# Kernel optimization log

Measured on AMD Instinct MI355X. Metric: run time of the kernel, lower is better.

Reference implementation:

```python
import jax, jax.numpy as jnp
import numpy as np

N_NODES = 100000
NODE_DIM = 64
IN_DIM_V = 128
N_LAYERS = 4
N_CLASSES = 40
N_EDGES = 1600000
LEAKY_SLOPE = 0.2
BN_EPS = 1e-5


def setup_inputs() -> dict:
    key = jax.random.key(0)
    ks = jax.random.split(key, 12)
    V = jax.random.normal(ks[0], (N_NODES, IN_DIM_V), dtype=jnp.float32)
    src = jax.random.randint(ks[1], (N_EDGES,), 0, N_NODES, dtype=jnp.int64 if jax.config.jax_enable_x64 else jnp.int32)
    dst = jax.random.randint(ks[2], (N_EDGES,), 0, N_NODES, dtype=jnp.int64 if jax.config.jax_enable_x64 else jnp.int32)
    s_in = 1.0 / np.sqrt(IN_DIM_V)
    s_h = 1.0 / np.sqrt(NODE_DIM)
    W_in = jax.random.normal(ks[3], (IN_DIM_V, NODE_DIM), dtype=jnp.float32) * s_in
    b_in = jnp.zeros((NODE_DIM,), jnp.float32)
    W_l = jax.random.normal(ks[4], (N_LAYERS, NODE_DIM, NODE_DIM), dtype=jnp.float32) * s_h
    b_l = jnp.zeros((N_LAYERS, NODE_DIM), jnp.float32)
    gamma = jnp.ones((N_LAYERS, NODE_DIM), jnp.float32)
    beta = jnp.zeros((N_LAYERS, NODE_DIM), jnp.float32)
    W_out = jax.random.normal(ks[5], (NODE_DIM, N_CLASSES), dtype=jnp.float32) * s_h
    b_out = jnp.zeros((N_CLASSES,), jnp.float32)
    return {"V": V, "src": src, "dst": dst, "W_in": W_in, "b_in": b_in,
            "W_l": W_l, "b_l": b_l, "gamma": gamma, "beta": beta,
            "W_out": W_out, "b_out": b_out}


def _batchnorm(x, g, b):
    # BatchNorm1d in training mode: biased variance over the node axis
    m = jnp.mean(x, axis=0)
    v = jnp.mean(jnp.square(x - m), axis=0)
    return (x - m) * jax.lax.rsqrt(v + BN_EPS) * g + b


def reference(V, src, dst, W_in, b_in, W_l, b_l, gamma, beta, W_out, b_out):
    N = V.shape[0]
    ones = jnp.ones((src.shape[0],), V.dtype)
    deg_out = jax.ops.segment_sum(ones, src, num_segments=N)
    deg_in = jax.ops.segment_sum(ones, dst, num_segments=N)
    norm_src = jax.lax.rsqrt(jnp.clip(deg_out, 1.0))[:, None]  # [N,1]
    norm_dst = jax.lax.rsqrt(jnp.clip(deg_in, 1.0))[:, None]

    # trans_input: linear embedding in_dim_V -> node_dim
    h = V @ W_in + b_in  # [N, node_dim]

    for l in range(N_LAYERS):
        h_in = h
        # dropout p=0 / eval mode -> identity
        # GraphConv norm='both': D^{-1/2} A D^{-1/2} X W + b
        m = h * norm_src                                      # [N, d]
        agg = jax.ops.segment_sum(m[src], dst, num_segments=N)  # gather-scatter over edges
        agg = agg * norm_dst
        hc = agg @ W_l[l] + b_l[l]
        hc = _batchnorm(hc, gamma[l], beta[l])
        hc = jnp.where(hc >= 0, hc, LEAKY_SLOPE * hc)
        h = hc + h_in  # residual (cell index hard-wired to 1 in source)

    logits = h @ W_out + b_out  # trans_output: node_dim -> n_classes
    return jax.nn.log_softmax(logits, axis=1)
```

## Files before the change

### kernel.cpp

```cpp
#include <hip/hip_runtime.h>
#include <math.h>


#define LEAKY_SLOPE 0.2f
#define BN_EPS 1e-5f
#define DEG_CAP 48

__device__ __forceinline__ unsigned short f2bf(float f) {
  unsigned int x = __float_as_uint(f);
  unsigned int r = (x + 0x7FFFu + ((x >> 16) & 1u)) >> 16;
  return (unsigned short)r;
}
__device__ __forceinline__ float bf2f(unsigned short u) {
  return __uint_as_float((unsigned int)u << 16);
}

__global__ __launch_bounds__(256, 8)
void hist_kernel(const int* __restrict__ src, int* __restrict__ cnt_src, int E, int N) {
  int bid = blockIdx.x;
  int w = bid & 7;
  int chunk = (N + 7) >> 3;
  int lo = w * chunk;
  int hi = min(lo + chunk, N);
  int i = (bid >> 3) * blockDim.x + threadIdx.x;
  int stride = (gridDim.x >> 3) * blockDim.x;
  for (; i < E; i += stride) {
    int s = src[i];
    if (s >= lo && s < hi) atomicAdd(&cnt_src[s], 1);
  }
}

__global__ __launch_bounds__(256, 8)
void fill_kernel(const int* __restrict__ src, const int* __restrict__ dst,
                 int* __restrict__ cnt_dst, int* __restrict__ bucket, int E, int N) {
  int bid = blockIdx.x;
  int w = bid & 7;
  int chunk = (N + 7) >> 3;
  int lo = w * chunk;
  int hi = min(lo + chunk, N);
  int i = (bid >> 3) * blockDim.x + threadIdx.x;
  int stride = (gridDim.x >> 3) * blockDim.x;
  for (; i < E; i += stride) {
    int d = dst[i];
    if (d >= lo && d < hi) {
      int pos = atomicAdd(&cnt_dst[d], 1);
      if (pos < DEG_CAP) bucket[d * DEG_CAP + pos] = src[i];
    }
  }
}

__global__ __launch_bounds__(256, 8)
void norms_kernel(const int* __restrict__ cnt_src, const int* __restrict__ cnt_dst,
                  float* __restrict__ norm_src, float* __restrict__ norm_dst, int N) {
  int i = blockIdx.x * blockDim.x + threadIdx.x;
  if (i < N) {
    norm_src[i] = rsqrtf(fmaxf((float)cnt_src[i], 1.0f));
    norm_dst[i] = rsqrtf(fmaxf((float)cnt_dst[i], 1.0f));
  }
}

__global__ __launch_bounds__(256) __attribute__((amdgpu_waves_per_eu(3, 4)))
void input_gemm_kernel(const float* __restrict__ V, const float* __restrict__ W_in,
                       const float* __restrict__ b_in, const float* __restrict__ norm_src,
                       float* __restrict__ h, unsigned short* __restrict__ hs, int N) {
  __shared__ __align__(16) float sW[128][64];
  __shared__ __align__(16) float sA[32][132];
  int tid = threadIdx.x;
  int c0 = (tid & 15) * 4;
  int rp = tid >> 4;
  int base = blockIdx.x * 32;

  float4 b4 = *(const float4*)&b_in[c0];

  #pragma unroll
  for (int it = 0; it < 8; it++) {
    int i = tid + it * 256;
    int r = i >> 4, cc = (i & 15) * 4;
    *(float4*)&sW[r][cc] = *(const float4*)&W_in[r * 64 + cc];
  }
  #pragma unroll
  for (int it = 0; it < 4; it++) {
    int i = tid + it * 256;
    int r = i >> 5, cc = (i & 31) * 4;
    int n = base + r;
    float4 v = make_float4(0.f, 0.f, 0.f, 0.f);
    if (n < N) v = *(const float4*)&V[(size_t)n * 128 + cc];
    *(float4*)&sA[r][cc] = v;
  }
  __syncthreads();

  int r0 = rp * 2, r1 = rp * 2 + 1;
  float acc0[4] = {0.f, 0.f, 0.f, 0.f};
  float acc1[4] = {0.f, 0.f, 0.f, 0.f};
  #pragma unroll 4
  for (int d0 = 0; d0 < 128; d0 += 4) {
    float4 wr0 = *(const float4*)&sW[d0 + 0][c0];
    float4 wr1 = *(const float4*)&sW[d0 + 1][c0];
    float4 wr2 = *(const float4*)&sW[d0 + 2][c0];
    float4 wr3 = *(const float4*)&sW[d0 + 3][c0];
    float4 a0 = *(const float4*)&sA[r0][d0];
    float4 a1 = *(const float4*)&sA[r1][d0];
    acc0[0] += a0.x * wr0.x + a0.y * wr1.x + a0.z * wr2.x + a0.w * wr3.x;
    acc0[1] += a0.x * wr0.y + a0.y * wr1.y + a0.z * wr2.y + a0.w * wr3.y;
    acc0[2] += a0.x * wr0.z + a0.y * wr1.z + a0.z * wr2.z + a0.w * wr3.z;
    acc0[3] += a0.x * wr0.w + a0.y * wr1.w + a0.z * wr2.w + a0.w * wr3.w;
    acc1[0] += a1.x * wr0.x + a1.y * wr1.x + a1.z * wr2.x + a1.w * wr3.x;
    acc1[1] += a1.x * wr0.y + a1.y * wr1.y + a1.z * wr2.y + a1.w * wr3.y;
    acc1[2] += a1.x * wr0.z + a1.y * wr1.z + a1.z * wr2.z + a1.w * wr3.z;
    acc1[3] += a1.x * wr0.w + a1.y * wr1.w + a1.z * wr2.w + a1.w * wr3.w;
  }

  int n0 = base + r0, n1 = base + r1;
  if (n0 < N) {
    float4 o = make_float4(acc0[0] + b4.x, acc0[1] + b4.y, acc0[2] + b4.z, acc0[3] + b4.w);
    *(float4*)&h[(size_t)n0 * 64 + c0] = o;
    float ns = norm_src[n0];
    ushort4 s = make_ushort4(f2bf(o.x * ns), f2bf(o.y * ns), f2bf(o.z * ns), f2bf(o.w * ns));
    *(ushort4*)&hs[(size_t)n0 * 64 + c0] = s;
  }
  if (n1 < N) {
    float4 o = make_float4(acc1[0] + b4.x, acc1[1] + b4.y, acc1[2] + b4.z, acc1[3] + b4.w);
    *(float4*)&h[(size_t)n1 * 64 + c0] = o;
    float ns = norm_src[n1];
    ushort4 s = make_ushort4(f2bf(o.x * ns), f2bf(o.y * ns), f2bf(o.z * ns), f2bf(o.w * ns));
    *(ushort4*)&hs[(size_t)n1 * 64 + c0] = s;
  }
}

__global__ __launch_bounds__(256, 8)
void agg_kernel(const unsigned short* __restrict__ hs, const float* __restrict__ norm_dst,
                const int* __restrict__ cnt_dst, const int* __restrict__ bucket,
                float* __restrict__ agg, int N) {
  int wid = __builtin_amdgcn_readfirstlane(blockIdx.x * 4 + (threadIdx.x >> 6));
  int lane = threadIdx.x & 63;
  if (wid >= N) return;
  int len = cnt_dst[wid];
  float nd = norm_dst[wid];
  const int* bkt = bucket + wid * DEG_CAP;
  float a0=0.f,a1=0.f,a2=0.f,a3=0.f,a4=0.f,a5=0.f,a6=0.f,a7=0.f;
  for (int j = 0; j < len; j += 8) {
    int s0=0,s1=0,s2=0,s3=0,s4=0,s5=0,s6=0,s7=0;
    if (j + 0 < len) s0 = bkt[j + 0];
    if (j + 1 < len) s1 = bkt[j + 1];
    if (j + 2 < len) s2 = bkt[j + 2];
    if (j + 3 < len) s3 = bkt[j + 3];
    if (j + 4 < len) s4 = bkt[j + 4];
    if (j + 5 < len) s5 = bkt[j + 5];
    if (j + 6 < len) s6 = bkt[j + 6];
    if (j + 7 < len) s7 = bkt[j + 7];
    unsigned short h0=0,h1=0,h2=0,h3=0,h4=0,h5=0,h6=0,h7=0;
    if (j + 0 < len) h0 = hs[(size_t)s0 * 64 + lane];
    if (j + 1 < len) h1 = hs[(size_t)s1 * 64 + lane];
    if (j + 2 < len) h2 = hs[(size_t)s2 * 64 + lane];
    if (j + 3 < len) h3 = hs[(size_t)s3 * 64 + lane];
    if (j + 4 < len) h4 = hs[(size_t)s4 * 64 + lane];
    if (j + 5 < len) h5 = hs[(size_t)s5 * 64 + lane];
    if (j + 6 < len) h6 = hs[(size_t)s6 * 64 + lane];
    if (j + 7 < len) h7 = hs[(size_t)s7 * 64 + lane];
    if (j + 0 < len) a0 += bf2f(h0);
    if (j + 1 < len) a1 += bf2f(h1);
    if (j + 2 < len) a2 += bf2f(h2);
    if (j + 3 < len) a3 += bf2f(h3);
    if (j + 4 < len) a4 += bf2f(h4);
    if (j + 5 < len) a5 += bf2f(h5);
    if (j + 6 < len) a6 += bf2f(h6);
    if (j + 7 < len) a7 += bf2f(h7);
  }
  float acc = ((a0 + a1) + (a2 + a3)) + ((a4 + a5) + (a6 + a7));
  agg[(size_t)wid * 64 + lane] = acc * nd;
}

__global__ __launch_bounds__(256) __attribute__((amdgpu_waves_per_eu(4, 4)))
void gemm_stats_kernel(const float* __restrict__ agg, const float* __restrict__ W,
                       const float* __restrict__ b, float* __restrict__ hc,
                       float* __restrict__ stats, int N) {
  __shared__ __align__(16) float sW[64][64];
  __shared__ __align__(16) float sA[64][68];
  int tid = threadIdx.x;
  int lane = tid & 63;
  int wv = tid >> 6;
  int cg = lane & 15;
  int ng = lane >> 4;
  int nrow0 = wv * 16 + ng * 4;
  int base = blockIdx.x * 64;

  #pragma unroll
  for (int it = 0; it < 4; it++) {
    int i = tid + it * 256;
    int r = i >> 4, c4 = (i & 15) * 4;
    *(float4*)&sW[r][c4] = *(const float4*)&W[r * 64 + c4];
  }
  #pragma unroll
  for (int it = 0; it < 4; it++) {
    int i = tid + it * 256;
    int r = i >> 4, c4 = (i & 15) * 4;
    int n = base + r;
    float4 v = make_float4(0.f, 0.f, 0.f, 0.f);
    if (n < N) v = *(const float4*)&agg[(size_t)n * 64 + c4];
    *(float4*)&sA[r][c4] = v;
  }
  __syncthreads();

  float4 b4 = *(const float4*)&b[cg * 4];

  float acc[4][4];
  #pragma unroll
  for (int i = 0; i < 4; i++)
    #pragma unroll
    for (int c = 0; c < 4; c++) acc[i][c] = 0.f;

  #pragma unroll 4
  for (int d0 = 0; d0 < 64; d0 += 4) {
    float4 wr0 = *(const float4*)&sW[d0 + 0][cg * 4];
    float4 wr1 = *(const float4*)&sW[d0 + 1][cg * 4];
    float4 wr2 = *(const float4*)&sW[d0 + 2][cg * 4];
    float4 wr3 = *(const float4*)&sW[d0 + 3][cg * 4];
    #pragma unroll
    for (int i = 0; i < 4; i++) {
      float4 av = *(const float4*)&sA[nrow0 + i][d0];
      acc[i][0] += av.x * wr0.x + av.y * wr1.x + av.z * wr2.x + av.w * wr3.x;
      acc[i][1] += av.x * wr0.y + av.y * wr1.y + av.z * wr2.y + av.w * wr3.y;
      acc[i][2] += av.x * wr0.z + av.y * wr1.z + av.z * wr2.z + av.w * wr3.z;
      acc[i][3] += av.x * wr0.w + av.y * wr1.w + av.z * wr2.w + av.w * wr3.w;
    }
  }

  float st_s0=0.f,st_s1=0.f,st_s2=0.f,st_s3=0.f;
  float st_q0=0.f,st_q1=0.f,st_q2=0.f,st_q3=0.f;
  #pragma unroll
  for (int i = 0; i < 4; i++) {
    int n = base + nrow0 + i;
    if (n < N) {
      float4 o;
      o.x = acc[i][0] + b4.x; o.y = acc[i][1] + b4.y;
      o.z = acc[i][2] + b4.z; o.w = acc[i][3] + b4.w;
      *(float4*)&hc[(size_t)n * 64 + cg * 4] = o;
      st_s0 += o.x; st_s1 += o.y; st_s2 += o.z; st_s3 += o.w;
      st_q0 += o.x * o.x; st_q1 += o.y * o.y;
      st_q2 += o.z * o.z; st_q3 += o.w * o.w;
    }
  }

  __syncthreads();
  int rr = wv * 4 + ng;
  *(float4*)&sA[rr][cg * 4]      = make_float4(st_s0, st_s1, st_s2, st_s3);
  *(float4*)&sA[16 + rr][cg * 4] = make_float4(st_q0, st_q1, st_q2, st_q3);
  __syncthreads();
  if (tid < 64) {
    float s = 0.f, q = 0.f;
    #pragma unroll
    for (int r = 0; r < 16; r++) { s += sA[r][tid]; q += sA[16 + r][tid]; }
    atomicAdd(&stats[tid], s);
    atomicAdd(&stats[64 + tid], q);
  }
}

__global__ __launch_bounds__(256, 8)
void apply_kernel(const float* __restrict__ hc, const float* __restrict__ stats,
                  const float* __restrict__ gamma, const float* __restrict__ beta,
                  const float* __restrict__ norm_src, float* __restrict__ h,
                  unsigned short* __restrict__ hs, int N, int write_hs) {
  __shared__ float s_scale[64];
  __shared__ float s_shift[64];
  int tid = threadIdx.x;
  if (tid < 64) {
    float s = stats[tid];
    float ss = stats[64 + tid];
    float invN = 1.0f / (float)N;
    float mean = s * invN;
    float var = fmaxf(ss * invN - mean * mean, 0.0f);
    float scale = gamma[tid] * rsqrtf(var + BN_EPS);
    s_scale[tid] = scale;
    s_shift[tid] = beta[tid] - mean * scale;
  }
  __syncthreads();
  int total4 = N * 16;
  int i = blockIdx.x * blockDim.x + threadIdx.x;
  int stride = gridDim.x * blockDim.x;
  for (; i < total4; i += stride) {
    float4 v = ((const float4*)hc)[i];
    float4 r = ((const float4*)h)[i];
    int cb = (i * 4) & 63;
    int n = i >> 4;
    float o0 = v.x * s_scale[cb + 0] + s_shift[cb + 0];
    float o1 = v.y * s_scale[cb + 1] + s_shift[cb + 1];
    float o2 = v.z * s_scale[cb + 2] + s_shift[cb + 2];
    float o3 = v.w * s_scale[cb + 3] + s_shift[cb + 3];
    o0 = (o0 >= 0.f) ? o0 : LEAKY_SLOPE * o0;
    o1 = (o1 >= 0.f) ? o1 : LEAKY_SLOPE * o1;
    o2 = (o2 >= 0.f) ? o2 : LEAKY_SLOPE * o2;
    o3 = (o3 >= 0.f) ? o3 : LEAKY_SLOPE * o3;
    float4 oh;
    oh.x = o0 + r.x; oh.y = o1 + r.y; oh.z = o2 + r.z; oh.w = o3 + r.w;
    ((float4*)h)[i] = oh;
    if (write_hs) {
      float nsc = norm_src[n];
      ushort4 os = make_ushort4(f2bf(oh.x * nsc), f2bf(oh.y * nsc),
                                f2bf(oh.z * nsc), f2bf(oh.w * nsc));
      ((ushort4*)hs)[i] = os;
    }
  }
}

__global__ __launch_bounds__(256, 4)
void out_kernel(const float* __restrict__ h, const float* __restrict__ W_out,
                const float* __restrict__ b_out, float* __restrict__ out, int N) {
  __shared__ float sWoT[40][65];
  int tid = threadIdx.x;
  for (int i = tid; i < 2560; i += 256) {
    int d = i / 40;
    int c = i - d * 40;
    sWoT[c][d] = W_out[i];
  }
  __syncthreads();
  int gw = (int)((blockIdx.x * blockDim.x + tid) >> 6);
  int nw = (int)((gridDim.x * blockDim.x) >> 6);
  int lane = tid & 63;
  int cc = (lane < 40) ? lane : 39;
  float bias = (lane < 40) ? b_out[lane] : 0.f;
  const float* wrow = &sWoT[cc][0];
  for (int n = gw; n < N; n += nw) {
    int nsg = __builtin_amdgcn_readfirstlane(n);
    const float* hrow = h + (size_t)nsg * 64;
    float acc = bias;
    #pragma unroll
    for (int d = 0; d < 64; d++) acc += hrow[d] * wrow[d];
    float lg = (lane < 40) ? acc : -INFINITY;
    float m = lg;
    #pragma unroll
    for (int off = 32; off; off >>= 1) m = fmaxf(m, __shfl_xor(m, off));
    float e = (lane < 40) ? expf(acc - m) : 0.f;
    float s = e;
    #pragma unroll
    for (int off = 32; off; off >>= 1) s += __shfl_xor(s, off);
    float lse = m + logf(s);
    if (lane < 40) out[(size_t)nsg * 40 + lane] = acc - lse;
  }
}

extern "C" void kernel_launch(void* const* d_in, const int* in_sizes, int n_in,
                              void* d_out, int out_size, void* d_ws, size_t ws_size,
                              hipStream_t stream) {
  const float* V     = (const float*)d_in[0];
  const int*   src   = (const int*)d_in[1];
  const int*   dst   = (const int*)d_in[2];
  const float* W_in  = (const float*)d_in[3];
  const float* b_in  = (const float*)d_in[4];
  const float* W_l   = (const float*)d_in[5];
  const float* b_l   = (const float*)d_in[6];
  const float* gamma = (const float*)d_in[7];
  const float* beta  = (const float*)d_in[8];
  const float* W_out = (const float*)d_in[9];
  const float* b_out = (const float*)d_in[10];
  float* out = (float*)d_out;

  const int N = in_sizes[0] / 128;
  const int E = in_sizes[1];
  const int NL = 4;

  char* p = (char*)d_ws;
  auto alloc = [&](size_t bytes) {
    void* r = (void*)p;
    p += (bytes + 255) & ~(size_t)255;
    return r;
  };
  float*          h       = (float*)alloc((size_t)N * 64 * 4);
  float*          agg     = (float*)alloc((size_t)N * 64 * 4);
  float*          hc      = (float*)alloc((size_t)N * 64 * 4);
  unsigned short* hs      = (unsigned short*)alloc((size_t)N * 64 * 2);
  int*            bucket  = (int*)alloc((size_t)N * DEG_CAP * 4);
  int*            cnt_src = (int*)alloc((size_t)N * 4);
  int*            cnt_dst = (int*)alloc((size_t)N * 4);
  float*          nrm_src = (float*)alloc((size_t)N * 4);
  float*          nrm_dst = (float*)alloc((size_t)N * 4);
  float*          stats   = (float*)alloc(128 * 4);
  (void)ws_size;

  hipMemsetAsync(cnt_src, 0, (size_t)N * 4, stream);
  hipMemsetAsync(cnt_dst, 0, (size_t)N * 4, stream);

  hist_kernel<<<2048, 256, 0, stream>>>(src, cnt_src, E, N);
  fill_kernel<<<2048, 256, 0, stream>>>(src, dst, cnt_dst, bucket, E, N);
  norms_kernel<<<(N + 255) / 256, 256, 0, stream>>>(cnt_src, cnt_dst, nrm_src, nrm_dst, N);

  input_gemm_kernel<<<(N + 31) / 32, 256, 0, stream>>>(V, W_in, b_in, nrm_src, h, hs, N);

  for (int l = 0; l < NL; l++) {
    agg_kernel<<<(N + 3) / 4, 256, 0, stream>>>(hs, nrm_dst, cnt_dst, bucket, agg, N);
    hipMemsetAsync(stats, 0, 128 * 4, stream);
    gemm_stats_kernel<<<(N + 63) / 64, 256, 0, stream>>>(agg, W_l + (size_t)l * 64 * 64,
                                                         b_l + (size_t)l * 64, hc, stats, N);
    apply_kernel<<<2048, 256, 0, stream>>>(hc, stats, gamma + (size_t)l * 64,
                                           beta + (size_t)l * 64, nrm_src, h, hs, N,
                                           (l < NL - 1) ? 1 : 0);
  }

  out_kernel<<<1024, 256, 0, stream>>>(h, W_out, b_out, out, N);
}
```

Before: 923.7 us.

## Fuse neighbor aggregation into GEMM+stats kernel, dropping agg buffer

Merges the per-layer gather aggregation into the GEMM/batchnorm-stats kernel. Each wave aggregates 16 destination rows directly into shared memory, with the two half-waves splitting the edges and each lane loading two bf16 values packed in one 32-bit word. This removes the fp32 agg round-trip through global memory and one launch per layer. In exchange there is less parallelism per row: each wave processes its rows one after another, and the kernel runs at the waves_per_eu(4,4) occupancy cap, so gather latency may be hidden less well.

Result: slower. 1.188 ms (+28.7%).

```diff
diff --git a/kernel.cpp b/kernel.cpp
--- a/kernel.cpp
+++ b/kernel.cpp
@@ -10,9 +10,6 @@
   unsigned int x = __float_as_uint(f);
   unsigned int r = (x + 0x7FFFu + ((x >> 16) & 1u)) >> 16;
   return (unsigned short)r;
-}
-__device__ __forceinline__ float bf2f(unsigned short u) {
-  return __uint_as_float((unsigned int)u << 16);
 }
 
 __global__ __launch_bounds__(256, 8)
@@ -127,61 +124,20 @@
   }
 }
 
-__global__ __launch_bounds__(256, 8)
-void agg_kernel(const unsigned short* __restrict__ hs, const float* __restrict__ norm_dst,
-                const int* __restrict__ cnt_dst, const int* __restrict__ bucket,
-                float* __restrict__ agg, int N) {
-  int wid = __builtin_amdgcn_readfirstlane(blockIdx.x * 4 + (threadIdx.x >> 6));
-  int lane = threadIdx.x & 63;
-  if (wid >= N) return;
-  int len = cnt_dst[wid];
-  float nd = norm_dst[wid];
-  const int* bkt = bucket + wid * DEG_CAP;
-  float a0=0.f,a1=0.f,a2=0.f,a3=0.f,a4=0.f,a5=0.f,a6=0.f,a7=0.f;
-  for (int j = 0; j < len; j += 8) {
-    int s0=0,s1=0,s2=0,s3=0,s4=0,s5=0,s6=0,s7=0;
-    if (j + 0 < len) s0 = bkt[j + 0];
-    if (j + 1 < len) s1 = bkt[j + 1];
-    if (j + 2 < len) s2 = bkt[j + 2];
-    if (j + 3 < len) s3 = bkt[j + 3];
-    if (j + 4 < len) s4 = bkt[j + 4];
-    if (j + 5 < len) s5 = bkt[j + 5];
-    if (j + 6 < len) s6 = bkt[j + 6];
-    if (j + 7 < len) s7 = bkt[j + 7];
-    unsigned short h0=0,h1=0,h2=0,h3=0,h4=0,h5=0,h6=0,h7=0;
-    if (j + 0 < len) h0 = hs[(size_t)s0 * 64 + lane];
-    if (j + 1 < len) h1 = hs[(size_t)s1 * 64 + lane];
-    if (j + 2 < len) h2 = hs[(size_t)s2 * 64 + lane];
-    if (j + 3 < len) h3 = hs[(size_t)s3 * 64 + lane];
-    if (j + 4 < len) h4 = hs[(size_t)s4 * 64 + lane];
-    if (j + 5 < len) h5 = hs[(size_t)s5 * 64 + lane];
-    if (j + 6 < len) h6 = hs[(size_t)s6 * 64 + lane];
-    if (j + 7 < len) h7 = hs[(size_t)s7 * 64 + lane];
-    if (j + 0 < len) a0 += bf2f(h0);
-    if (j + 1 < len) a1 += bf2f(h1);
-    if (j + 2 < len) a2 += bf2f(h2);
-    if (j + 3 < len) a3 += bf2f(h3);
-    if (j + 4 < len) a4 += bf2f(h4);
-    if (j + 5 < len) a5 += bf2f(h5);
-    if (j + 6 < len) a6 += bf2f(h6);
-    if (j + 7 < len) a7 += bf2f(h7);
-  }
-  float acc = ((a0 + a1) + (a2 + a3)) + ((a4 + a5) + (a6 + a7));
-  agg[(size_t)wid * 64 + lane] = acc * nd;
-}
-
 __global__ __launch_bounds__(256) __attribute__((amdgpu_waves_per_eu(4, 4)))
-void gemm_stats_kernel(const float* __restrict__ agg, const float* __restrict__ W,
-                       const float* __restrict__ b, float* __restrict__ hc,
-                       float* __restrict__ stats, int N) {
+void agg_gemm_stats_kernel(const unsigned short* __restrict__ hs,
+                           const float* __restrict__ norm_dst,
+                           const int* __restrict__ cnt_dst,
+                           const int* __restrict__ bucket,
+                           const float* __restrict__ W, const float* __restrict__ b,
+                           float* __restrict__ hc, float* __restrict__ stats, int N) {
   __shared__ __align__(16) float sW[64][64];
   __shared__ __align__(16) float sA[64][68];
   int tid = threadIdx.x;
   int lane = tid & 63;
   int wv = tid >> 6;
-  int cg = lane & 15;
-  int ng = lane >> 4;
-  int nrow0 = wv * 16 + ng * 4;
+  int half = lane >> 5;
+  int l = lane & 31;
   int base = blockIdx.x * 64;
 
   #pragma unroll
@@ -190,16 +146,41 @@
     int r = i >> 4, c4 = (i & 15) * 4;
     *(float4*)&sW[r][c4] = *(const float4*)&W[r * 64 + c4];
   }
-  #pragma unroll
-  for (int it = 0; it < 4; it++) {
-    int i = tid + it * 256;
-    int r = i >> 4, c4 = (i & 15) * 4;
+
+  for (int i = 0; i < 16; i++) {
+    int r = wv * 16 + i;
     int n = base + r;
-    float4 v = make_float4(0.f, 0.f, 0.f, 0.f);
-    if (n < N) v = *(const float4*)&agg[(size_t)n * 64 + c4];
-    *(float4*)&sA[r][c4] = v;
-  }
-  __syncthreads();
+    float acc0 = 0.f, acc1 = 0.f;
+    if (n < N) {
+      int len = min(cnt_dst[n], DEG_CAP);
+      const int* bkt = bucket + (size_t)n * DEG_CAP;
+      for (int j = 0; j < len; j += 16) {
+        #pragma unroll
+        for (int k = 0; k < 8; k++) {
+          int e = j + 2 * k + half;
+          if (e < len) {
+            int sidx = bkt[e];
+            unsigned int u = *(const unsigned int*)&hs[(size_t)sidx * 64 + 2 * l];
+            acc0 += __uint_as_float(u << 16);
+            acc1 += __uint_as_float(u & 0xFFFF0000u);
+          }
+        }
+      }
+      acc0 += __shfl_xor(acc0, 32);
+      acc1 += __shfl_xor(acc1, 32);
+      float nd = norm_dst[n];
+      acc0 *= nd; acc1 *= nd;
+    }
+    if (half == 0) {
+      sA[r][2 * l]     = acc0;
+      sA[r][2 * l + 1] = acc1;
+    }
+  }
+  __syncthreads();
+
+  int cg = lane & 15;
+  int ng = lane >> 4;
+  int nrow0 = wv * 16 + ng * 4;
 
   float4 b4 = *(const float4*)&b[cg * 4];
 
@@ -365,7 +346,6 @@
     return r;
   };
   float*          h       = (float*)alloc((size_t)N * 64 * 4);
-  float*          agg     = (float*)alloc((size_t)N * 64 * 4);
   float*          hc      = (float*)alloc((size_t)N * 64 * 4);
   unsigned short* hs      = (unsigned short*)alloc((size_t)N * 64 * 2);
   int*            bucket  = (int*)alloc((size_t)N * DEG_CAP * 4);
@@ -386,10 +366,10 @@
   input_gemm_kernel<<<(N + 31) / 32, 256, 0, stream>>>(V, W_in, b_in, nrm_src, h, hs, N);
 
   for (int l = 0; l < NL; l++) {
-    agg_kernel<<<(N + 3) / 4, 256, 0, stream>>>(hs, nrm_dst, cnt_dst, bucket, agg, N);
     hipMemsetAsync(stats, 0, 128 * 4, stream);
-    gemm_stats_kernel<<<(N + 63) / 64, 256, 0, stream>>>(agg, W_l + (size_t)l * 64 * 64,
-                                                         b_l + (size_t)l * 64, hc, stats, N);
+    agg_gemm_stats_kernel<<<(N + 63) / 64, 256, 0, stream>>>(
+        hs, nrm_dst, cnt_dst, bucket, W_l + (size_t)l * 64 * 64,
+        b_l + (size_t)l * 64, hc, stats, N);
     apply_kernel<<<2048, 256, 0, stream>>>(hc, stats, gamma + (size_t)l * 64,
                                            beta + (size_t)l * 64, nrm_src, h, hs, N,
                                            (l < NL - 1) ? 1 : 0);
```
